# Performance work log

Measured on AMD Instinct MI355X. Metric: run time of the kernel, lower is better.

The kernel has to match this reference:

```python
import jax, jax.numpy as jnp
import numpy as np

B, IN, H, HEADS, W, P = 512, 512, 1024, 16, 32, 64
EPS = 1e-5

def _pe(w, p, dtype=jnp.float32):
    # sinusoidal positional encoding over the attention window, [w, p]
    pos = jnp.arange(w, dtype=dtype)[:, None]
    div = jnp.exp(-jnp.arange(0, p, 2, dtype=dtype) * (np.log(10000.0) / p))
    ang = pos * div[None, :]
    pe = jnp.zeros((w, p), dtype)
    pe = pe.at[:, 0::2].set(jnp.sin(ang))
    pe = pe.at[:, 1::2].set(jnp.cos(ang))
    return pe

def _bn(x, g, b, m, v):
    # BatchNorm1d in eval mode (running stats)
    return (x - m) * (g / jnp.sqrt(v + EPS)) + b

def setup_inputs():
    key = jax.random.key(0)
    ks = iter(jax.random.split(key, 40))
    s = 1.0 / np.sqrt(H)  # init_parameters('pytorch_default'): U(-1/sqrt(H), 1/sqrt(H))
    u = lambda shape: jax.random.uniform(next(ks), shape, jnp.float32, -s, s)
    rn = lambda shape: jax.random.normal(next(ks), shape, jnp.float32)
    return {
        "x": rn((B, IN)),
        "prev_hidden": rn((B, H)),
        "prev_cell": rn((B, H)),
        "past_cells": rn((W, B, H)),
        "W_ih": u((4 * H, IN)), "b_ih": u((4 * H,)),
        "W_hh": u((4 * H, H)),
        "W_q": u((H, IN + H)), "b_q": u((H,)),
        "W_ac": u((4 * H, H)), "b_ac": u((4 * H,)),
        "Wq_a": u((H, H)), "bq_a": u((H,)),
        "Wk_a": u((H, H + P)), "bk_a": u((H,)),
        "Wv_a": u((H, H + P)), "bv_a": u((H,)),
        "Wo_a": u((H, H)), "bo_a": u((H,)),
        "bn_attn_gamma": u((H,)), "bn_attn_beta": u((H,)),
        "bn_attn_mean": jnp.zeros((H,)), "bn_attn_var": jnp.ones((H,)),
        "bn_post_gamma": u((H,)), "bn_post_beta": u((H,)),
        "bn_post_mean": jnp.zeros((H,)), "bn_post_var": jnp.ones((H,)),
    }

def reference(x, prev_hidden, prev_cell, past_cells, W_ih, b_ih, W_hh, W_q, b_q, W_ac, b_ac, Wq_a, bq_a, Wk_a, bk_a, Wv_a, bv_a, Wo_a, bo_a, bn_attn_gamma, bn_attn_beta, bn_attn_mean, bn_attn_var, bn_post_gamma, bn_post_beta, bn_post_mean, bn_post_var):
    dk = H // HEADS
    # Q = elu(Wq * concat(x, h) + b)
    q = jax.nn.elu(jnp.concatenate([x, prev_hidden], -1) @ W_q.T + b_q)      # [B,H]
    # K = V = window of past cell states (+ positional encoding on features)
    vals = jnp.transpose(past_cells, (1, 0, 2))                              # [B,W,H]
    pe = jnp.broadcast_to(_pe(W, P)[None], (vals.shape[0], W, P))
    kv = jnp.concatenate([vals, pe], -1)                                     # [B,W,H+P]
    Q = (q @ Wq_a.T + bq_a).reshape(-1, HEADS, dk)                           # [B,h,dk]
    K = jax.nn.elu(kv @ Wk_a.T + bk_a).reshape(-1, W, HEADS, dk)             # activation_on_keys_and_values
    V = jax.nn.elu(kv @ Wv_a.T + bv_a).reshape(-1, W, HEADS, dk)
    scores = jnp.einsum('bhd,bwhd->bhw', Q, K) / np.sqrt(dk)
    ctx = jnp.einsum('bhw,bwhd->bhd', jax.nn.softmax(scores, -1), V).reshape(-1, H)
    attn = jax.nn.elu(ctx @ Wo_a.T + bo_a)                                   # [B,H]
    attn = _bn(attn, bn_attn_gamma, bn_attn_beta, bn_attn_mean, bn_attn_var)
    # 'residual' mode: Wx*x + Wh*h + Wa*a + b  (note: original returns pre-BN value)
    pre = x @ W_ih.T + b_ih + prev_hidden @ W_hh.T + attn @ W_ac.T + b_ac    # [B,4H]
    iv = jnp.tanh(pre[:, :H])
    gates = jax.nn.sigmoid(pre[:, H:])
    f, i, o = gates[:, :H], gates[:, H:2 * H], gates[:, 2 * H:]
    cell = iv * i + prev_cell * f
    hidden = _bn(o * jax.nn.elu(cell), bn_post_gamma, bn_post_beta, bn_post_mean, bn_post_var)
    return hidden
```

## Files before the change

kernel.cpp:

```cpp
#include <hip/hip_runtime.h>
#include <hip/hip_bf16.h>

typedef __attribute__((ext_vector_type(8))) short s16x8;
typedef __attribute__((ext_vector_type(8))) unsigned short u16x8;
typedef __attribute__((ext_vector_type(4))) float f32x4;

__device__ __forceinline__ float bf2f(unsigned short u) {
  union { unsigned int i; float f; } v; v.i = ((unsigned int)u) << 16; return v.f;
}
__device__ __forceinline__ unsigned short f2bf(float f) {
  union { float f; unsigned int i; } v; v.f = f;
  unsigned int u = v.i;
  unsigned int r = (u + 0x7fffu + ((u >> 16) & 1u)) >> 16;
  return (unsigned short)r;
}
__device__ __forceinline__ float eluf(float x) { return x > 0.f ? x : expf(x) - 1.f; }
__device__ __forceinline__ float sigf(float x) { return 1.f / (1.f + expf(-x)); }

__device__ __forceinline__ void gl_lds16(const unsigned short* g, unsigned short* l) {
  __builtin_amdgcn_global_load_lds(
      (const __attribute__((address_space(1))) void*)g,
      (__attribute__((address_space(3))) void*)l, 16, 0, 0);
}

__global__ __launch_bounds__(256)
void cast_all(const float* __restrict__ pcs,
              const float* __restrict__ W_ih, const float* __restrict__ W_hh,
              const float* __restrict__ W_ac, const float* __restrict__ W_q,
              const float* __restrict__ Wq_a, const float* __restrict__ Wo_a,
              const float* __restrict__ Wk_a, const float* __restrict__ Wv_a,
              const float* __restrict__ x, const float* __restrict__ ph,
              unsigned short* __restrict__ A_pc, unsigned short* __restrict__ W6,
              unsigned short* __restrict__ Wq, unsigned short* __restrict__ Wqa,
              unsigned short* __restrict__ Woa, unsigned short* __restrict__ Wkv,
              unsigned short* __restrict__ A6) {
  int c = blockIdx.x * 256 + threadIdx.x;
  const float* src; unsigned short* dst; int row, col, ldd;
  if (c < 2097152) {
    row = c >> 7; col = (c & 127) << 3;
    src = pcs + (size_t)row * 1024 + col; dst = A_pc; ldd = 1024;
  } else if (c < 3407872) {
    int i = c - 2097152; row = i / 320; col = (i - row * 320) << 3;
    dst = W6; ldd = 2560;
    src = (col < 512)  ? W_ih + (size_t)row * 512 + col
        : (col < 1536) ? W_hh + (size_t)row * 1024 + (col - 512)
                       : W_ac + (size_t)row * 1024 + (col - 1536);
  } else if (c < 3604480) {
    int i = c - 3407872; row = i / 192; col = (i - row * 192) << 3;
    src = W_q + (size_t)row * 1536 + col; dst = Wq; ldd = 1536;
  } else if (c < 3735552) {
    int i = c - 3604480; row = i >> 7; col = (i & 127) << 3;
    src = Wq_a + (size_t)row * 1024 + col; dst = Wqa; ldd = 1024;
  } else if (c < 3866624) {
    int i = c - 3735552; row = i >> 7; col = (i & 127) << 3;
    src = Wo_a + (size_t)row * 1024 + col; dst = Woa; ldd = 1024;
  } else if (c < 4128768) {
    int i = c - 3866624; row = i >> 7; col = (i & 127) << 3;
    src = (row < 1024) ? Wk_a + (size_t)row * 1088 + col
                       : Wv_a + (size_t)(row - 1024) * 1088 + col;
    dst = Wkv; ldd = 1024;
  } else {
    int i = c - 4128768; row = i / 192; col = (i - row * 192) << 3;
    src = (col < 512) ? x + (size_t)row * 512 + col
                      : ph + (size_t)row * 1024 + (col - 512);
    dst = A6; ldd = 2560;
  }
  f32x4 v0 = *(const f32x4*)src;
  f32x4 v1 = *(const f32x4*)(src + 4);
  u16x8 r;
  r[0] = f2bf(v0.x); r[1] = f2bf(v0.y); r[2] = f2bf(v0.z); r[3] = f2bf(v0.w);
  r[4] = f2bf(v1.x); r[5] = f2bf(v1.y); r[6] = f2bf(v1.z); r[7] = f2bf(v1.w);
  int sc = col ^ ((row & 7) << 3);
  *(u16x8*)(dst + (size_t)row * ldd + sc) = r;
}

struct GP2 {
  const unsigned short* A; long lda;
  const unsigned short* B; long ldb;
  const float* bias; const float* peb;
  const float* bnS; const float* bnT;
  float* of; unsigned short* ob; unsigned short* ob2;
  int N, K;
};

template<int BM, int BN, int EPI, int PEB, int ACT>
__global__ __launch_bounds__(256)
void gemm2(GP2 p) {
  __shared__ unsigned short sA[BM * 64];
  __shared__ unsigned short sB[BN * 64];
  const int tid = threadIdx.x, lane = tid & 63, wid = tid >> 6;
  const int col0 = blockIdx.x * BN, row0 = blockIdx.y * BM;
  constexpr int WRS = BM / 2, WCS = BN / 2;
  constexpr int MI = WRS / 16, NI = WCS / 16;
  const int wr = (wid >> 1) * WRS, wc = (wid & 1) * WCS;
  const int g = lane >> 4, lr = lane & 15;
  f32x4 acc[MI][NI] = {};

  for (int kb = 0; kb < p.K; kb += 64) {
    __syncthreads();
#pragma unroll
    for (int ps = 0; ps < (BM * 8) / 256; ++ps) {
      int chunk = ps * 256 + wid * 64 + lane;
      int r = chunk >> 3, c8 = chunk & 7;
      gl_lds16(p.A + (size_t)(row0 + r) * p.lda + kb + c8 * 8, &sA[chunk * 8]);
    }
#pragma unroll
    for (int ps = 0; ps < (BN * 8) / 256; ++ps) {
      int chunk = ps * 256 + wid * 64 + lane;
      int r = chunk >> 3, c8 = chunk & 7;
      gl_lds16(p.B + (size_t)(col0 + r) * p.ldb + kb + c8 * 8, &sB[chunk * 8]);
    }
    __syncthreads();
#pragma unroll
    for (int kk = 0; kk < 64; kk += 32) {
      s16x8 af[MI], bf_[NI];
#pragma unroll
      for (int i = 0; i < MI; ++i) {
        int ar = wr + i * 16 + lr;
        int sl = ((kk >> 3) + g) ^ (ar & 7);
        af[i] = *(const s16x8*)(&sA[(ar * 8 + sl) * 8]);
      }
#pragma unroll
      for (int i = 0; i < NI; ++i) {
        int br = wc + i * 16 + lr;
        int sl = ((kk >> 3) + g) ^ (br & 7);
        bf_[i] = *(const s16x8*)(&sB[(br * 8 + sl) * 8]);
      }
#pragma unroll
      for (int mi = 0; mi < MI; ++mi)
#pragma unroll
        for (int ni = 0; ni < NI; ++ni)
          acc[mi][ni] = __builtin_amdgcn_mfma_f32_16x16x32_bf16(
              af[mi], bf_[ni], acc[mi][ni], 0, 0, 0);
    }
  }

#pragma unroll
  for (int mi = 0; mi < MI; ++mi) {
#pragma unroll
    for (int ni = 0; ni < NI; ++ni) {
#pragma unroll
      for (int rg = 0; rg < 4; ++rg) {
        int rr = row0 + wr + mi * 16 + g * 4 + rg;
        int cc = col0 + wc + ni * 16 + lr;
        float v = acc[mi][ni][rg];
        if constexpr (PEB) v += p.peb[(size_t)(rr >> 9) * 2048 + cc];
        else v += p.bias[cc];
        if constexpr (ACT) v = eluf(v);
        if constexpr (EPI == 0) {
          p.of[(size_t)rr * p.N + cc] = v;
        } else if constexpr (EPI == 1) {
          p.ob[(size_t)rr * p.N + (cc ^ ((rr & 7) << 3))] = f2bf(v);
        } else if constexpr (EPI == 2) {
          if (cc < 1024) p.ob[(size_t)rr * 1024 + cc] = f2bf(v);
          else           p.ob2[(size_t)rr * 1024 + (cc - 1024)] = f2bf(v);
        } else {
          v = v * p.bnS[cc] + p.bnT[cc];
          p.ob[(size_t)rr * 2560 + ((1536 + cc) ^ ((rr & 7) << 3))] = f2bf(v);
        }
      }
    }
  }
}

__global__ __launch_bounds__(256)
void prep_peb(const float* __restrict__ Wk, const float* __restrict__ Wv,
              const float* __restrict__ bk, const float* __restrict__ bv,
              float* __restrict__ peb) {
  int idx = blockIdx.x * 256 + threadIdx.x;
  int w = idx >> 11, n = idx & 2047;
  const float* Wrow =
      ((n < 1024) ? (Wk + (size_t)n * 1088) : (Wv + (size_t)(n - 1024) * 1088)) + 1024;
  float acc = (n < 1024) ? bk[n] : bv[n - 1024];
  const float c0 = logf(10000.f) / 64.f;
#pragma unroll
  for (int j = 0; j < 32; ++j) {
    float ang = (float)w * __expf(-(2.f * j) * c0);
    acc += __sinf(ang) * Wrow[2 * j] + __cosf(ang) * Wrow[2 * j + 1];
  }
  peb[idx] = acc;
}

__global__ void prep_misc(const float* b_ih, const float* b_ac,
                          const float* g1, const float* be1, const float* m1, const float* v1,
                          const float* g2, const float* be2, const float* m2, const float* v2,
                          float* bias6, float* s1, float* t1, float* s2, float* t2) {
  int i = blockIdx.x * 256 + threadIdx.x;
  if (i < 4096) bias6[i] = b_ih[i] + b_ac[i];
  if (i < 1024) {
    float sa = g1[i] * rsqrtf(v1[i] + 1e-5f);
    s1[i] = sa; t1[i] = be1[i] - m1[i] * sa;
    float sp = g2[i] * rsqrtf(v2[i] + 1e-5f);
    s2[i] = sp; t2[i] = be2[i] - m2[i] * sp;
  }
}

__global__ __launch_bounds__(256)
void attn_k(const float* __restrict__ Q, const unsigned short* __restrict__ Kb,
            const unsigned short* __restrict__ Vb, unsigned short* __restrict__ ctx) {
  int lane = threadIdx.x & 63;
  int gw = (blockIdx.x << 2) + (threadIdx.x >> 6);
  int b = gw >> 4, h = gw & 15;
  int w = lane & 31, half = lane >> 5;
  const unsigned short* Krow = Kb + (size_t)(w * 512 + b) * 1024 + h * 64 + half * 32;
  const float* Qp = Q + (size_t)b * 1024 + h * 64 + half * 32;
  float s = 0.f;
#pragma unroll
  for (int j = 0; j < 32; j += 8) {
    u16x8 kv = *(const u16x8*)(Krow + j);
    f32x4 q0 = *(const f32x4*)(Qp + j);
    f32x4 q1 = *(const f32x4*)(Qp + j + 4);
    s += q0.x * bf2f(kv[0]) + q0.y * bf2f(kv[1]) + q0.z * bf2f(kv[2]) + q0.w * bf2f(kv[3])
       + q1.x * bf2f(kv[4]) + q1.y * bf2f(kv[5]) + q1.z * bf2f(kv[6]) + q1.w * bf2f(kv[7]);
  }
  s += __shfl_xor(s, 32);
  s *= 0.125f;
  float mx = s;
#pragma unroll
  for (int off = 16; off; off >>= 1) mx = fmaxf(mx, __shfl_xor(mx, off));
  float e = expf(s - mx);
  float sum = e;
#pragma unroll
  for (int off = 16; off; off >>= 1) sum += __shfl_xor(sum, off);
  float pr = e / sum;
  float c = 0.f;
#pragma unroll 8
  for (int w2 = 0; w2 < 32; ++w2) {
    float pw = __shfl(pr, w2);
    c += pw * bf2f(Vb[(size_t)(w2 * 512 + b) * 1024 + h * 64 + lane]);
  }
  ctx[(size_t)b * 1024 + ((h * 64 + lane) ^ ((b & 7) << 3))] = f2bf(c);
}

__global__ __launch_bounds__(256)
void final_k(const float* __restrict__ pre, const float* __restrict__ pcell,
             const float* __restrict__ s2, const float* __restrict__ t2,
             float* __restrict__ out) {
  int i = blockIdx.x * 256 + threadIdx.x;
  int j = i & 1023;
  const float* pm = pre + (size_t)(i >> 10) * 4096;
  float iv = tanhf(pm[j]);
  float f  = sigf(pm[1024 + j]);
  float ii = sigf(pm[2048 + j]);
  float o  = sigf(pm[3072 + j]);
  float cell = iv * ii + pcell[i] * f;
  float ec = cell > 0.f ? cell : expf(cell) - 1.f;
  out[i] = (o * ec) * s2[j] + t2[j];
}

extern "C" void kernel_launch(void* const* d_in, const int* in_sizes, int n_in,
                              void* d_out, int out_size, void* d_ws, size_t ws_size,
                              hipStream_t stream) {
  (void)in_sizes; (void)n_in; (void)out_size; (void)ws_size;
  const float* x     = (const float*)d_in[0];
  const float* ph    = (const float*)d_in[1];
  const float* pcell = (const float*)d_in[2];
  const float* pcs   = (const float*)d_in[3];
  const float* W_ih  = (const float*)d_in[4];
  const float* b_ih  = (const float*)d_in[5];
  const float* W_hh  = (const float*)d_in[6];
  const float* W_q   = (const float*)d_in[7];
  const float* b_q   = (const float*)d_in[8];
  const float* W_ac  = (const float*)d_in[9];
  const float* b_ac  = (const float*)d_in[10];
  const float* Wq_a  = (const float*)d_in[11];
  const float* bq_a  = (const float*)d_in[12];
  const float* Wk_a  = (const float*)d_in[13];
  const float* bk_a  = (const float*)d_in[14];
  const float* Wv_a  = (const float*)d_in[15];
  const float* bv_a  = (const float*)d_in[16];
  const float* Wo_a  = (const float*)d_in[17];
  const float* bo_a  = (const float*)d_in[18];
  const float* g1    = (const float*)d_in[19];
  const float* be1   = (const float*)d_in[20];
  const float* m1    = (const float*)d_in[21];
  const float* v1    = (const float*)d_in[22];
  const float* g2    = (const float*)d_in[23];
  const float* be2   = (const float*)d_in[24];
  const float* m2    = (const float*)d_in[25];
  const float* v2    = (const float*)d_in[26];

  char* wp = (char*)d_ws;
  auto alloc = [&](size_t bytes) {
    char* r = wp; wp += (bytes + 255) & ~(size_t)255; return r;
  };
  unsigned short* A_pc  = (unsigned short*)alloc((size_t)16384 * 1024 * 2);
  unsigned short* W6    = (unsigned short*)alloc((size_t)4096 * 2560 * 2);
  unsigned short* Wq    = (unsigned short*)alloc((size_t)1024 * 1536 * 2);
  unsigned short* Wqa   = (unsigned short*)alloc((size_t)1024 * 1024 * 2);
  unsigned short* Woa   = (unsigned short*)alloc((size_t)1024 * 1024 * 2);
  unsigned short* Wkv   = (unsigned short*)alloc((size_t)2048 * 1024 * 2);
  unsigned short* A6    = (unsigned short*)alloc((size_t)512 * 2560 * 2);
  unsigned short* q_bf  = (unsigned short*)alloc((size_t)512 * 1024 * 2);
  float*          Qf    = (float*)alloc((size_t)512 * 1024 * 4);
  unsigned short* K_bf  = (unsigned short*)alloc((size_t)16384 * 1024 * 2);
  unsigned short* V_bf  = (unsigned short*)alloc((size_t)16384 * 1024 * 2);
  unsigned short* ctxbf = (unsigned short*)alloc((size_t)512 * 1024 * 2);
  float*          pre   = (float*)alloc((size_t)512 * 4096 * 4);
  float*          peb   = (float*)alloc((size_t)32 * 2048 * 4);
  float*          bias6 = (float*)alloc((size_t)4096 * 4);
  float*          s1    = (float*)alloc((size_t)1024 * 4);
  float*          t1    = (float*)alloc((size_t)1024 * 4);
  float*          s2    = (float*)alloc((size_t)1024 * 4);
  float*          t2    = (float*)alloc((size_t)1024 * 4);

  cast_all<<<16512, 256, 0, stream>>>(pcs, W_ih, W_hh, W_ac, W_q, Wq_a, Wo_a,
                                      Wk_a, Wv_a, x, ph,
                                      A_pc, W6, Wq, Wqa, Woa, Wkv, A6);
  prep_peb<<<256, 256, 0, stream>>>(Wk_a, Wv_a, bk_a, bv_a, peb);
  prep_misc<<<16, 256, 0, stream>>>(b_ih, b_ac, g1, be1, m1, v1, g2, be2, m2, v2,
                                    bias6, s1, t1, s2, t2);

  {
    GP2 p = {};
    p.A = A_pc; p.lda = 1024; p.B = Wkv; p.ldb = 1024;
    p.peb = peb; p.ob = K_bf; p.ob2 = V_bf; p.N = 2048; p.K = 1024;
    gemm2<128, 128, 2, 1, 1><<<dim3(16, 128), 256, 0, stream>>>(p);
  }
  {
    GP2 p = {};
    p.A = A6; p.lda = 2560; p.B = Wq; p.ldb = 1536;
    p.bias = b_q; p.ob = q_bf; p.N = 1024; p.K = 1536;
    gemm2<64, 64, 1, 0, 1><<<dim3(16, 8), 256, 0, stream>>>(p);
  }
  {
    GP2 p = {};
    p.A = q_bf; p.lda = 1024; p.B = Wqa; p.ldb = 1024;
    p.bias = bq_a; p.of = Qf; p.N = 1024; p.K = 1024;
    gemm2<64, 64, 0, 0, 0><<<dim3(16, 8), 256, 0, stream>>>(p);
  }
  attn_k<<<2048, 256, 0, stream>>>(Qf, K_bf, V_bf, ctxbf);
  {
    GP2 p = {};
    p.A = ctxbf; p.lda = 1024; p.B = Woa; p.ldb = 1024;
    p.bias = bo_a; p.bnS = s1; p.bnT = t1; p.ob = A6; p.N = 1024; p.K = 1024;
    gemm2<64, 64, 3, 0, 1><<<dim3(16, 8), 256, 0, stream>>>(p);
  }
  {
    GP2 p = {};
    p.A = A6; p.lda = 2560; p.B = W6; p.ldb = 2560;
    p.bias = bias6; p.of = pre; p.N = 4096; p.K = 2560;
    gemm2<128, 128, 0, 0, 0><<<dim3(32, 4), 256, 0, stream>>>(p);
  }
  final_k<<<2048, 256, 0, stream>>>(pre, pcell, s2, t2, (float*)d_out);
}
```

Measured before the change: 415.4 us.

## Fuse K/V projection GEMM with windowed attention and merge prep kernels

Attention now runs inside the K/V projection GEMM. Each block computes K and V for 4 batch rows × one head over all 32 window positions, keeps them in LDS and does softmax and context there. This removes writing and re-reading the large bf16 K and V tensors (16384×1024 each) through global memory. The small prep kernels (positional bias, BN scale and shift, bias sums) are folded into the cast kernel to save launches, fast exp/tanh intrinsics replace the libm calls, and the final gate GEMM uses 64×128 tiles for more blocks. The risk is that the fused tile layout, with rows interleaved by window position, has poorer A-load coalescing, and the fast math loses a little accuracy.

Result: faster. 381.1 us (-8.2%).

```diff
diff --git a/kernel.cpp b/kernel.cpp
--- a/kernel.cpp
+++ b/kernel.cpp
@@ -14,8 +14,14 @@
   unsigned int r = (u + 0x7fffu + ((u >> 16) & 1u)) >> 16;
   return (unsigned short)r;
 }
-__device__ __forceinline__ float eluf(float x) { return x > 0.f ? x : expf(x) - 1.f; }
-__device__ __forceinline__ float sigf(float x) { return 1.f / (1.f + expf(-x)); }
+__device__ __forceinline__ float eluf(float x) { return x > 0.f ? x : __expf(x) - 1.f; }
+__device__ __forceinline__ float sigf(float x) { return 1.f / (1.f + __expf(-x)); }
+__device__ __forceinline__ float tanhfast(float x) {
+  float ax = fminf(fabsf(x), 15.f);
+  float e2 = __expf(2.f * ax);
+  float t = (e2 - 1.f) / (e2 + 1.f);
+  return x < 0.f ? -t : t;
+}
 
 __device__ __forceinline__ void gl_lds16(const unsigned short* g, unsigned short* l) {
   __builtin_amdgcn_global_load_lds(
@@ -23,47 +29,71 @@
       (__attribute__((address_space(3))) void*)l, 16, 0, 0);
 }
 
+struct CP {
+  const float *pcs, *W_ih, *W_hh, *W_ac, *W_q, *Wq_a, *Wo_a, *Wk_a, *Wv_a, *x, *ph;
+  const float *b_ih, *b_ac, *bk, *bv;
+  const float *g1, *be1, *m1, *v1, *g2, *be2, *m2, *v2;
+  unsigned short *A_pc, *W6, *Wq, *Wqa, *Woa, *Wkv, *A6;
+  float *peb, *bias6, *s1, *t1, *s2, *t2;
+};
+
 __global__ __launch_bounds__(256)
-void cast_all(const float* __restrict__ pcs,
-              const float* __restrict__ W_ih, const float* __restrict__ W_hh,
-              const float* __restrict__ W_ac, const float* __restrict__ W_q,
-              const float* __restrict__ Wq_a, const float* __restrict__ Wo_a,
-              const float* __restrict__ Wk_a, const float* __restrict__ Wv_a,
-              const float* __restrict__ x, const float* __restrict__ ph,
-              unsigned short* __restrict__ A_pc, unsigned short* __restrict__ W6,
-              unsigned short* __restrict__ Wq, unsigned short* __restrict__ Wqa,
-              unsigned short* __restrict__ Woa, unsigned short* __restrict__ Wkv,
-              unsigned short* __restrict__ A6) {
+void cast_all(CP p) {
   int c = blockIdx.x * 256 + threadIdx.x;
   const float* src; unsigned short* dst; int row, col, ldd;
   if (c < 2097152) {
     row = c >> 7; col = (c & 127) << 3;
-    src = pcs + (size_t)row * 1024 + col; dst = A_pc; ldd = 1024;
+    src = p.pcs + (size_t)row * 1024 + col; dst = p.A_pc; ldd = 1024;
   } else if (c < 3407872) {
     int i = c - 2097152; row = i / 320; col = (i - row * 320) << 3;
-    dst = W6; ldd = 2560;
-    src = (col < 512)  ? W_ih + (size_t)row * 512 + col
-        : (col < 1536) ? W_hh + (size_t)row * 1024 + (col - 512)
-                       : W_ac + (size_t)row * 1024 + (col - 1536);
+    dst = p.W6; ldd = 2560;
+    src = (col < 512)  ? p.W_ih + (size_t)row * 512 + col
+        : (col < 1536) ? p.W_hh + (size_t)row * 1024 + (col - 512)
+                       : p.W_ac + (size_t)row * 1024 + (col - 1536);
   } else if (c < 3604480) {
     int i = c - 3407872; row = i / 192; col = (i - row * 192) << 3;
-    src = W_q + (size_t)row * 1536 + col; dst = Wq; ldd = 1536;
+    src = p.W_q + (size_t)row * 1536 + col; dst = p.Wq; ldd = 1536;
   } else if (c < 3735552) {
     int i = c - 3604480; row = i >> 7; col = (i & 127) << 3;
-    src = Wq_a + (size_t)row * 1024 + col; dst = Wqa; ldd = 1024;
+    src = p.Wq_a + (size_t)row * 1024 + col; dst = p.Wqa; ldd = 1024;
   } else if (c < 3866624) {
     int i = c - 3735552; row = i >> 7; col = (i & 127) << 3;
-    src = Wo_a + (size_t)row * 1024 + col; dst = Woa; ldd = 1024;
+    src = p.Wo_a + (size_t)row * 1024 + col; dst = p.Woa; ldd = 1024;
   } else if (c < 4128768) {
     int i = c - 3866624; row = i >> 7; col = (i & 127) << 3;
-    src = (row < 1024) ? Wk_a + (size_t)row * 1088 + col
-                       : Wv_a + (size_t)(row - 1024) * 1088 + col;
-    dst = Wkv; ldd = 1024;
+    src = (row < 1024) ? p.Wk_a + (size_t)row * 1088 + col
+                       : p.Wv_a + (size_t)(row - 1024) * 1088 + col;
+    dst = p.Wkv; ldd = 1024;
+  } else if (c < 4227072) {
+    int i = c - 4128768; row = i / 192; col = (i - row * 192) << 3;
+    src = (col < 512) ? p.x + (size_t)row * 512 + col
+                      : p.ph + (size_t)row * 1024 + (col - 512);
+    dst = p.A6; ldd = 2560;
+  } else if (c < 4292608) {
+    int idx = c - 4227072;
+    int w = idx >> 11, n = idx & 2047;
+    const float* Wrow =
+        ((n < 1024) ? (p.Wk_a + (size_t)n * 1088)
+                    : (p.Wv_a + (size_t)(n - 1024) * 1088)) + 1024;
+    float accv = (n < 1024) ? p.bk[n] : p.bv[n - 1024];
+    const float c0 = 0.14391157f;
+#pragma unroll
+    for (int j = 0; j < 32; ++j) {
+      float ang = (float)w * __expf(-(2.f * j) * c0);
+      accv += __sinf(ang) * Wrow[2 * j] + __cosf(ang) * Wrow[2 * j + 1];
+    }
+    p.peb[idx] = accv;
+    return;
   } else {
-    int i = c - 4128768; row = i / 192; col = (i - row * 192) << 3;
-    src = (col < 512) ? x + (size_t)row * 512 + col
-                      : ph + (size_t)row * 1024 + (col - 512);
-    dst = A6; ldd = 2560;
+    int i = c - 4292608;
+    if (i < 4096) p.bias6[i] = p.b_ih[i] + p.b_ac[i];
+    if (i < 1024) {
+      float sa = p.g1[i] * rsqrtf(p.v1[i] + 1e-5f);
+      p.s1[i] = sa; p.t1[i] = p.be1[i] - p.m1[i] * sa;
+      float sp = p.g2[i] * rsqrtf(p.v2[i] + 1e-5f);
+      p.s2[i] = sp; p.t2[i] = p.be2[i] - p.m2[i] * sp;
+    }
+    return;
   }
   f32x4 v0 = *(const f32x4*)src;
   f32x4 v1 = *(const f32x4*)(src + 4);
@@ -77,13 +107,13 @@
 struct GP2 {
   const unsigned short* A; long lda;
   const unsigned short* B; long ldb;
-  const float* bias; const float* peb;
+  const float* bias;
   const float* bnS; const float* bnT;
-  float* of; unsigned short* ob; unsigned short* ob2;
+  float* of; unsigned short* ob;
   int N, K;
 };
 
-template<int BM, int BN, int EPI, int PEB, int ACT>
+template<int BM, int BN, int EPI, int ACT>
 __global__ __launch_bounds__(256)
 void gemm2(GP2 p) {
   __shared__ unsigned short sA[BM * 64];
@@ -100,13 +130,13 @@
     __syncthreads();
 #pragma unroll
     for (int ps = 0; ps < (BM * 8) / 256; ++ps) {
-      int chunk = ps * 256 + wid * 64 + lane;
+      int chunk = ps * 256 + tid;
       int r = chunk >> 3, c8 = chunk & 7;
       gl_lds16(p.A + (size_t)(row0 + r) * p.lda + kb + c8 * 8, &sA[chunk * 8]);
     }
 #pragma unroll
     for (int ps = 0; ps < (BN * 8) / 256; ++ps) {
-      int chunk = ps * 256 + wid * 64 + lane;
+      int chunk = ps * 256 + tid;
       int r = chunk >> 3, c8 = chunk & 7;
       gl_lds16(p.B + (size_t)(col0 + r) * p.ldb + kb + c8 * 8, &sB[chunk * 8]);
     }
@@ -143,17 +173,12 @@
       for (int rg = 0; rg < 4; ++rg) {
         int rr = row0 + wr + mi * 16 + g * 4 + rg;
         int cc = col0 + wc + ni * 16 + lr;
-        float v = acc[mi][ni][rg];
-        if constexpr (PEB) v += p.peb[(size_t)(rr >> 9) * 2048 + cc];
-        else v += p.bias[cc];
+        float v = acc[mi][ni][rg] + p.bias[cc];
         if constexpr (ACT) v = eluf(v);
         if constexpr (EPI == 0) {
           p.of[(size_t)rr * p.N + cc] = v;
         } else if constexpr (EPI == 1) {
           p.ob[(size_t)rr * p.N + (cc ^ ((rr & 7) << 3))] = f2bf(v);
-        } else if constexpr (EPI == 2) {
-          if (cc < 1024) p.ob[(size_t)rr * 1024 + cc] = f2bf(v);
-          else           p.ob2[(size_t)rr * 1024 + (cc - 1024)] = f2bf(v);
         } else {
           v = v * p.bnS[cc] + p.bnT[cc];
           p.ob[(size_t)rr * 2560 + ((1536 + cc) ^ ((rr & 7) << 3))] = f2bf(v);
@@ -164,72 +189,122 @@
 }
 
 __global__ __launch_bounds__(256)
-void prep_peb(const float* __restrict__ Wk, const float* __restrict__ Wv,
-              const float* __restrict__ bk, const float* __restrict__ bv,
-              float* __restrict__ peb) {
-  int idx = blockIdx.x * 256 + threadIdx.x;
-  int w = idx >> 11, n = idx & 2047;
-  const float* Wrow =
-      ((n < 1024) ? (Wk + (size_t)n * 1088) : (Wv + (size_t)(n - 1024) * 1088)) + 1024;
-  float acc = (n < 1024) ? bk[n] : bv[n - 1024];
-  const float c0 = logf(10000.f) / 64.f;
-#pragma unroll
-  for (int j = 0; j < 32; ++j) {
-    float ang = (float)w * __expf(-(2.f * j) * c0);
-    acc += __sinf(ang) * Wrow[2 * j] + __cosf(ang) * Wrow[2 * j + 1];
-  }
-  peb[idx] = acc;
-}
-
-__global__ void prep_misc(const float* b_ih, const float* b_ac,
-                          const float* g1, const float* be1, const float* m1, const float* v1,
-                          const float* g2, const float* be2, const float* m2, const float* v2,
-                          float* bias6, float* s1, float* t1, float* s2, float* t2) {
-  int i = blockIdx.x * 256 + threadIdx.x;
-  if (i < 4096) bias6[i] = b_ih[i] + b_ac[i];
-  if (i < 1024) {
-    float sa = g1[i] * rsqrtf(v1[i] + 1e-5f);
-    s1[i] = sa; t1[i] = be1[i] - m1[i] * sa;
-    float sp = g2[i] * rsqrtf(v2[i] + 1e-5f);
-    s2[i] = sp; t2[i] = be2[i] - m2[i] * sp;
-  }
-}
-
-__global__ __launch_bounds__(256)
-void attn_k(const float* __restrict__ Q, const unsigned short* __restrict__ Kb,
-            const unsigned short* __restrict__ Vb, unsigned short* __restrict__ ctx) {
-  int lane = threadIdx.x & 63;
-  int gw = (blockIdx.x << 2) + (threadIdx.x >> 6);
-  int b = gw >> 4, h = gw & 15;
-  int w = lane & 31, half = lane >> 5;
-  const unsigned short* Krow = Kb + (size_t)(w * 512 + b) * 1024 + h * 64 + half * 32;
-  const float* Qp = Q + (size_t)b * 1024 + h * 64 + half * 32;
+void gkv_attn(const unsigned short* __restrict__ A_pc,
+              const unsigned short* __restrict__ Wkv,
+              const float* __restrict__ peb,
+              const float* __restrict__ Qf,
+              unsigned short* __restrict__ ctx) {
+  __shared__ unsigned short smem[2 * 128 * 64];
+  __shared__ float prs[4][32];
+  __shared__ float qs[4][64];
+  unsigned short* sA = smem;
+  unsigned short* sB = smem + 128 * 64;
+
+  int id = blockIdx.x;
+  int nid = (id & 7) * 256 + (id >> 3);
+  const int h = nid & 15, bg = nid >> 4;
+  const int b0 = bg * 4;
+
+  const int tid = threadIdx.x, lane = tid & 63, wid = tid >> 6;
+  const int wr = (wid >> 1) * 64, wc = (wid & 1) * 64;
+  const int g = lane >> 4, lr = lane & 15;
+  f32x4 acc[4][4] = {};
+
+  for (int kb = 0; kb < 1024; kb += 64) {
+    __syncthreads();
+#pragma unroll
+    for (int ps = 0; ps < 4; ++ps) {
+      int chunk = ps * 256 + tid;
+      int r = chunk >> 3, c8 = chunk & 7;
+      int w = r >> 2;
+      int srow = w * 512 + b0 + (r & 3);
+      int xf = (r & 7) ^ (srow & 7);
+      gl_lds16(A_pc + (size_t)srow * 1024 + kb + ((c8 ^ xf) << 3), &sA[chunk * 8]);
+    }
+#pragma unroll
+    for (int ps = 0; ps < 4; ++ps) {
+      int chunk = ps * 256 + tid;
+      int r = chunk >> 3, c8 = chunk & 7;
+      int n = h * 64 + r + (r >= 64 ? 960 : 0);
+      gl_lds16(Wkv + (size_t)n * 1024 + kb + (c8 << 3), &sB[chunk * 8]);
+    }
+    __syncthreads();
+#pragma unroll
+    for (int kk = 0; kk < 64; kk += 32) {
+      s16x8 af[4], bf_[4];
+#pragma unroll
+      for (int i = 0; i < 4; ++i) {
+        int ar = wr + i * 16 + lr;
+        int sl = ((kk >> 3) + g) ^ (ar & 7);
+        af[i] = *(const s16x8*)(&sA[(ar * 8 + sl) * 8]);
+        int br = wc + i * 16 + lr;
+        int sl2 = ((kk >> 3) + g) ^ (br & 7);
+        bf_[i] = *(const s16x8*)(&sB[(br * 8 + sl2) * 8]);
+      }
+#pragma unroll
+      for (int mi = 0; mi < 4; ++mi)
+#pragma unroll
+        for (int ni = 0; ni < 4; ++ni)
+          acc[mi][ni] = __builtin_amdgcn_mfma_f32_16x16x32_bf16(
+              af[mi], bf_[ni], acc[mi][ni], 0, 0, 0);
+    }
+  }
+  __syncthreads();
+
+  unsigned short (*kv)[128] = (unsigned short(*)[128])smem;
+#pragma unroll
+  for (int mi = 0; mi < 4; ++mi) {
+#pragma unroll
+    for (int ni = 0; ni < 4; ++ni) {
+#pragma unroll
+      for (int rg = 0; rg < 4; ++rg) {
+        int rr = wr + mi * 16 + g * 4 + rg;
+        int cc = wc + ni * 16 + lr;
+        int w = rr >> 2;
+        int gcol = h * 64 + cc + (cc >= 64 ? 960 : 0);
+        float v = acc[mi][ni][rg] + peb[w * 2048 + gcol];
+        v = v > 0.f ? v : __expf(v) - 1.f;
+        kv[rr][cc ^ ((rr & 7) << 3)] = f2bf(v);
+      }
+    }
+  }
+  qs[wid][lane] = Qf[(size_t)(b0 + wid) * 1024 + h * 64 + lane];
+  __syncthreads();
+
+  const int wv = wid;
+  const int w = lane & 31, half = lane >> 5;
   float s = 0.f;
-#pragma unroll
-  for (int j = 0; j < 32; j += 8) {
-    u16x8 kv = *(const u16x8*)(Krow + j);
-    f32x4 q0 = *(const f32x4*)(Qp + j);
-    f32x4 q1 = *(const f32x4*)(Qp + j + 4);
-    s += q0.x * bf2f(kv[0]) + q0.y * bf2f(kv[1]) + q0.z * bf2f(kv[2]) + q0.w * bf2f(kv[3])
-       + q1.x * bf2f(kv[4]) + q1.y * bf2f(kv[5]) + q1.z * bf2f(kv[6]) + q1.w * bf2f(kv[7]);
+  {
+    int r = w * 4 + wv;
+    int swz = r & 7;
+#pragma unroll
+    for (int jj = 0; jj < 4; ++jj) {
+      u16x8 kx = *(const u16x8*)(&kv[r][((half * 4 + jj) ^ swz) << 3]);
+#pragma unroll
+      for (int e = 0; e < 8; ++e)
+        s += qs[wv][half * 32 + jj * 8 + e] * bf2f(kx[e]);
+    }
   }
   s += __shfl_xor(s, 32);
   s *= 0.125f;
   float mx = s;
 #pragma unroll
   for (int off = 16; off; off >>= 1) mx = fmaxf(mx, __shfl_xor(mx, off));
-  float e = expf(s - mx);
+  float e = __expf(s - mx);
   float sum = e;
 #pragma unroll
   for (int off = 16; off; off >>= 1) sum += __shfl_xor(sum, off);
-  float pr = e / sum;
+  if (lane < 32) prs[wv][lane] = e / sum;
+
   float c = 0.f;
+  const int d = lane;
 #pragma unroll 8
   for (int w2 = 0; w2 < 32; ++w2) {
-    float pw = __shfl(pr, w2);
-    c += pw * bf2f(Vb[(size_t)(w2 * 512 + b) * 1024 + h * 64 + lane]);
-  }
-  ctx[(size_t)b * 1024 + ((h * 64 + lane) ^ ((b & 7) << 3))] = f2bf(c);
+    int r = w2 * 4 + wv;
+    c += prs[wv][w2] * bf2f(kv[r][(64 + d) ^ ((r & 7) << 3)]);
+  }
+  int b = b0 + wv;
+  ctx[(size_t)b * 1024 + ((h * 64 + d) ^ ((b & 7) << 3))] = f2bf(c);
 }
 
 __global__ __launch_bounds__(256)
@@ -239,12 +314,12 @@
   int i = blockIdx.x * 256 + threadIdx.x;
   int j = i & 1023;
   const float* pm = pre + (size_t)(i >> 10) * 4096;
-  float iv = tanhf(pm[j]);
+  float iv = tanhfast(pm[j]);
   float f  = sigf(pm[1024 + j]);
   float ii = sigf(pm[2048 + j]);
   float o  = sigf(pm[3072 + j]);
   float cell = iv * ii + pcell[i] * f;
-  float ec = cell > 0.f ? cell : expf(cell) - 1.f;
+  float ec = cell > 0.f ? cell : __expf(cell) - 1.f;
   out[i] = (o * ec) * s2[j] + t2[j];
 }
 
@@ -271,14 +346,6 @@
   const float* bv_a  = (const float*)d_in[16];
   const float* Wo_a  = (const float*)d_in[17];
   const float* bo_a  = (const float*)d_in[18];
-  const float* g1    = (const float*)d_in[19];
-  const float* be1   = (const float*)d_in[20];
-  const float* m1    = (const float*)d_in[21];
-  const float* v1    = (const float*)d_in[22];
-  const float* g2    = (const float*)d_in[23];
-  const float* be2   = (const float*)d_in[24];
-  const float* m2    = (const float*)d_in[25];
-  const float* v2    = (const float*)d_in[26];
 
   char* wp = (char*)d_ws;
   auto alloc = [&](size_t bytes) {
@@ -293,8 +360,6 @@
   unsigned short* A6    = (unsigned short*)alloc((size_t)512 * 2560 * 2);
   unsigned short* q_bf  = (unsigned short*)alloc((size_t)512 * 1024 * 2);
   float*          Qf    = (float*)alloc((size_t)512 * 1024 * 4);
-  unsigned short* K_bf  = (unsigned short*)alloc((size_t)16384 * 1024 * 2);
-  unsigned short* V_bf  = (unsigned short*)alloc((size_t)16384 * 1024 * 2);
   unsigned short* ctxbf = (unsigned short*)alloc((size_t)512 * 1024 * 2);
   float*          pre   = (float*)alloc((size_t)512 * 4096 * 4);
   float*          peb   = (float*)alloc((size_t)32 * 2048 * 4);
@@ -304,43 +369,46 @@
   float*          s2    = (float*)alloc((size_t)1024 * 4);
   float*          t2    = (float*)alloc((size_t)1024 * 4);
 
-  cast_all<<<16512, 256, 0, stream>>>(pcs, W_ih, W_hh, W_ac, W_q, Wq_a, Wo_a,
-                                      Wk_a, Wv_a, x, ph,
-                                      A_pc, W6, Wq, Wqa, Woa, Wkv, A6);
-  prep_peb<<<256, 256, 0, stream>>>(Wk_a, Wv_a, bk_a, bv_a, peb);
-  prep_misc<<<16, 256, 0, stream>>>(b_ih, b_ac, g1, be1, m1, v1, g2, be2, m2, v2,
-                                    bias6, s1, t1, s2, t2);
-
-  {
-    GP2 p = {};
-    p.A = A_pc; p.lda = 1024; p.B = Wkv; p.ldb = 1024;
-    p.peb = peb; p.ob = K_bf; p.ob2 = V_bf; p.N = 2048; p.K = 1024;
-    gemm2<128, 128, 2, 1, 1><<<dim3(16, 128), 256, 0, stream>>>(p);
-  }
+  {
+    CP cp = {};
+    cp.pcs = pcs; cp.W_ih = W_ih; cp.W_hh = W_hh; cp.W_ac = W_ac; cp.W_q = W_q;
+    cp.Wq_a = Wq_a; cp.Wo_a = Wo_a; cp.Wk_a = Wk_a; cp.Wv_a = Wv_a;
+    cp.x = x; cp.ph = ph;
+    cp.b_ih = b_ih; cp.b_ac = b_ac; cp.bk = bk_a; cp.bv = bv_a;
+    cp.g1 = (const float*)d_in[19]; cp.be1 = (const float*)d_in[20];
+    cp.m1 = (const float*)d_in[21]; cp.v1 = (const float*)d_in[22];
+    cp.g2 = (const float*)d_in[23]; cp.be2 = (const float*)d_in[24];
+    cp.m2 = (const float*)d_in[25]; cp.v2 = (const float*)d_in[26];
+    cp.A_pc = A_pc; cp.W6 = W6; cp.Wq = Wq; cp.Wqa = Wqa; cp.Woa = Woa;
+    cp.Wkv = Wkv; cp.A6 = A6;
+    cp.peb = peb; cp.bias6 = bias6; cp.s1 = s1; cp.t1 = t1; cp.s2 = s2; cp.t2 = t2;
+    cast_all<<<16784, 256, 0, stream>>>(cp);
+  }
+
   {
     GP2 p = {};
     p.A = A6; p.lda = 2560; p.B = Wq; p.ldb = 1536;
     p.bias = b_q; p.ob = q_bf; p.N = 1024; p.K = 1536;
-    gemm2<64, 64, 1, 0, 1><<<dim3(16, 8), 256, 0, stream>>>(p);
+    gemm2<64, 64, 1, 1><<<dim3(16, 8), 256, 0, stream>>>(p);
   }
   {
     GP2 p = {};
     p.A = q_bf; p.lda = 1024; p.B = Wqa; p.ldb = 1024;
     p.bias = bq_a; p.of = Qf; p.N = 1024; p.K = 1024;
-    gemm2<64, 64, 0, 0, 0><<<dim3(16, 8), 256, 0, stream>>>(p);
-  }
-  attn_k<<<2048, 256, 0, stream>>>(Qf, K_bf, V_bf, ctxbf);
+    gemm2<64, 64, 0, 0><<<dim3(16, 8), 256, 0, stream>>>(p);
+  }
+  gkv_attn<<<2048, 256, 0, stream>>>(A_pc, Wkv, peb, Qf, ctxbf);
   {
     GP2 p = {};
     p.A = ctxbf; p.lda = 1024; p.B = Woa; p.ldb = 1024;
     p.bias = bo_a; p.bnS = s1; p.bnT = t1; p.ob = A6; p.N = 1024; p.K = 1024;
-    gemm2<64, 64, 3, 0, 1><<<dim3(16, 8), 256, 0, stream>>>(p);
+    gemm2<64, 64, 3, 1><<<dim3(16, 8), 256, 0, stream>>>(p);
   }
   {
     GP2 p = {};
     p.A = A6; p.lda = 2560; p.B = W6; p.ldb = 2560;
     p.bias = bias6; p.of = pre; p.N = 4096; p.K = 2560;
-    gemm2<128, 128, 0, 0, 0><<<dim3(32, 4), 256, 0, stream>>>(p);
+    gemm2<64, 128, 0, 0><<<dim3(32, 8), 256, 0, stream>>>(p);
   }
   final_k<<<2048, 256, 0, stream>>>(pre, pcell, s2, t2, (float*)d_out);
 }
```
